# Optimization experiments

Hardware: AMD Instinct MI355X
Metric: run time of the kernel (lower is better)

Reference implementation:

```python
import jax, jax.numpy as jnp
import numpy as np

N_NODES = 50000
N_EDGES = 800000
IN_C = 32
HID = 64
N_LAYERS = 3
EDGE_HID = 128
OUT_C = 1
N_GRAPHS = 8


def setup_inputs() -> dict:
    key = jax.random.key(0)
    ks = jax.random.split(key, 32)
    x = jax.random.normal(ks[0], (N_NODES, IN_C), dtype=jnp.float32)
    # edges with src != dst so that PyG's remove_self_loops is a no-op
    src = jax.random.randint(ks[1], (N_EDGES,), 0, N_NODES)
    off = jax.random.randint(ks[2], (N_EDGES,), 1, N_NODES)
    dst = (src + off) % N_NODES
    edge_index = jnp.stack([src, dst]).astype(jnp.int32)
    batch = jnp.sort(jax.random.randint(ks[3], (N_NODES,), 0, N_GRAPHS)).astype(jnp.int32)
    inp = {"x": x, "edge_index": edge_index, "batch": batch}
    i = 4
    for l in range(N_LAYERS):
        din = IN_C if l == 0 else HID
        s = 1.0 / float(np.sqrt(din))
        inp[f"Wl{l}"] = jax.random.normal(ks[i], (din, HID), dtype=jnp.float32) * s; i += 1
        inp[f"bl{l}"] = jnp.zeros((HID,), jnp.float32)
        inp[f"Wr{l}"] = jax.random.normal(ks[i], (din, HID), dtype=jnp.float32) * s; i += 1
        inp[f"br{l}"] = jnp.zeros((HID,), jnp.float32)
        inp[f"att{l}"] = jax.random.normal(ks[i], (HID,), dtype=jnp.float32) * (1.0 / float(np.sqrt(HID))); i += 1
        inp[f"res{l}"] = jax.random.normal(ks[i], (din, HID), dtype=jnp.float32) * s; i += 1
        inp[f"bias{l}"] = jnp.zeros((HID,), jnp.float32)
        inp[f"lng{l}"] = jnp.ones((HID,), jnp.float32)
        inp[f"lnb{l}"] = jnp.zeros((HID,), jnp.float32)
    efd = 3 * HID
    inp["W1"] = jax.random.normal(ks[i], (efd, EDGE_HID), dtype=jnp.float32) * (1.0 / float(np.sqrt(efd))); i += 1
    inp["b1"] = jnp.zeros((EDGE_HID,), jnp.float32)
    inp["W2"] = jax.random.normal(ks[i], (EDGE_HID, OUT_C), dtype=jnp.float32) * (1.0 / float(np.sqrt(EDGE_HID))); i += 1
    inp["b2"] = jnp.zeros((OUT_C,), jnp.float32)
    return inp


def _gatv2_layer(x, src, dst, Wl, bl, Wr, br, att, resW, bias):
    # GATv2Conv (heads=1, share_weights=False, residual=True, add_self_loops handled by caller)
    n = x.shape[0]
    xl = x @ Wl + bl  # source transform  [N, C]
    xr = x @ Wr + br  # target transform  [N, C]
    e = jax.nn.leaky_relu(xl[src] + xr[dst], 0.2)  # [E, C]
    logits = e @ att                               # [E]
    m = jax.ops.segment_max(logits, dst, num_segments=n)
    ex = jnp.exp(logits - m[dst])
    denom = jax.ops.segment_sum(ex, dst, num_segments=n)
    alpha = ex / denom[dst]                        # edge softmax over incoming edges
    out = jax.ops.segment_sum(alpha[:, None] * xl[src], dst, num_segments=n)
    return out + x @ resW + bias


def _layernorm(h, g, b):
    mu = h.mean(-1, keepdims=True)
    var = h.var(-1, keepdims=True)
    return (h - mu) * jax.lax.rsqrt(var + 1e-5) * g + b


def reference(x, edge_index, batch,
              Wl0, bl0, Wr0, br0, att0, res0, bias0, lng0, lnb0,
              Wl1, bl1, Wr1, br1, att1, res1, bias1, lng1, lnb1,
              Wl2, bl2, Wr2, br2, att2, res2, bias2, lng2, lnb2,
              W1, b1, W2, b2):
    n = x.shape[0]
    loop = jnp.arange(n, dtype=edge_index.dtype)
    src = jnp.concatenate([edge_index[0], loop])  # add self loops
    dst = jnp.concatenate([edge_index[1], loop])
    layers = [(Wl0, bl0, Wr0, br0, att0, res0, bias0, lng0, lnb0),
              (Wl1, bl1, Wr1, br1, att1, res1, bias1, lng1, lnb1),
              (Wl2, bl2, Wr2, br2, att2, res2, bias2, lng2, lnb2)]
    h = x
    for (Wl, bl, Wr, br, att, resW, bias, g, b) in layers:
        h = _gatv2_layer(h, src, dst, Wl, bl, Wr, br, att, resW, bias)
        h = jax.nn.relu(_layernorm(h, g, b))
    node_repr = h
    gc = jax.ops.segment_sum(node_repr, batch, num_segments=N_GRAPHS)  # global_add_pool
    s, d = edge_index[0], edge_index[1]
    edge_feat = jnp.concatenate([node_repr[s], node_repr[d], gc[batch[s]]], axis=-1)  # [E, 3*HID]
    return jax.nn.relu(edge_feat @ W1 + b1) @ W2 + b2
```

## Files before the change

### kernel.cpp

```cpp
#include <hip/hip_runtime.h>
#include <math.h>

typedef float floatx2 __attribute__((ext_vector_type(2)));
typedef float floatx4 __attribute__((ext_vector_type(4)));
typedef short bf16x8 __attribute__((ext_vector_type(8)));
typedef _Float16 halfx2 __attribute__((ext_vector_type(2)));

#define NODE_MASK 0x07FFFFFF
#define LOG2E 1.4426950408889634f

__device__ __forceinline__ float wave_sum(float v){
#pragma unroll
  for (int m = 1; m < 64; m <<= 1) v += __shfl_xor(v, m, 64);
  return v;
}

__device__ __forceinline__ unsigned short bf16_of(float a){
  unsigned ua = __float_as_uint(a);
  ua = (ua + 0x7FFFu + ((ua >> 16) & 1u)) >> 16;
  return (unsigned short)ua;
}
__device__ __forceinline__ unsigned pack_bf16(float a, float b){
  unsigned ua = __float_as_uint(a), ub = __float_as_uint(b);
  ua = (ua + 0x7FFFu + ((ua >> 16) & 1u)) >> 16;
  ub = (ub + 0x7FFFu + ((ub >> 16) & 1u)) >> 16;
  return ua | (ub << 16);
}
__device__ __forceinline__ float2 unpack_bf16(unsigned p){
  float2 r;
  r.x = __uint_as_float(p << 16);
  r.y = __uint_as_float(p & 0xFFFF0000u);
  return r;
}
__device__ __forceinline__ bf16x8 to_bf16x8(float4 a, float4 b){
  bf16x8 r;
  r[0]=(short)bf16_of(a.x); r[1]=(short)bf16_of(a.y);
  r[2]=(short)bf16_of(a.z); r[3]=(short)bf16_of(a.w);
  r[4]=(short)bf16_of(b.x); r[5]=(short)bf16_of(b.y);
  r[6]=(short)bf16_of(b.z); r[7]=(short)bf16_of(b.w);
  return r;
}
__device__ __forceinline__ halfx2 f22h2(float a, float b){
  auto r = __builtin_amdgcn_cvt_pkrtz(a, b);
  return *(halfx2*)&r;
}
__device__ __forceinline__ float fdot2h(halfx2 a, halfx2 b, float c){
  return __builtin_amdgcn_fdot2(a, b, c, false);
}

__global__ __launch_bounds__(256)
void k_deg_t0(const int* __restrict__ dst, int* __restrict__ deg, int* __restrict__ rank, int e,
              const float* __restrict__ h,
              const float* __restrict__ Wl, const float* __restrict__ bl,
              const float* __restrict__ Wr, const float* __restrict__ br,
              const float* __restrict__ Wres, const float* __restrict__ bias,
              unsigned short* __restrict__ xl8, float* __restrict__ xr,
              float* __restrict__ res, int n, int nt64){
  if ((int)blockIdx.x >= nt64){
    int c = blockIdx.x - nt64;
    int i = (c*256 + (int)threadIdx.x)*4;
    if (i + 3 < e){
      int4 d4 = *(const int4*)&dst[i];
      int4 r4;
      r4.x = atomicAdd(&deg[d4.x], 1);
      r4.y = atomicAdd(&deg[d4.y], 1);
      r4.z = atomicAdd(&deg[d4.z], 1);
      r4.w = atomicAdd(&deg[d4.w], 1);
      *(int4*)&rank[i] = r4;
    } else {
      for (int j = i; j < e; ++j) rank[j] = atomicAdd(&deg[dst[j]], 1);
    }
    return;
  }
  const int K = 32, KH = 1;
  int lane = threadIdx.x & 63;
  int nt   = threadIdx.x >> 6;
  int nn = lane & 15, q = lane >> 4;
  int m0 = blockIdx.x * 64;
  if (m0 >= n) return;
  bf16x8 Af[4][KH];
#pragma unroll
  for (int t = 0; t < 4; ++t){
#pragma unroll
    for (int kh = 0; kh < KH; ++kh){
      int node = min(m0 + t*16 + nn, n - 1);
      const float* hp = h + (size_t)node*K + kh*32 + q*8;
      Af[t][kh] = to_bf16x8(*(const float4*)hp, *(const float4*)(hp + 4));
    }
  }
  int n0 = nt * 16;
  for (int sel = 0; sel < 3; ++sel){
    const float* Wp = (sel == 0) ? Wl : (sel == 1) ? Wr : Wres;
    const float* bp = (sel == 0) ? bl : (sel == 1) ? br : bias;
    bf16x8 Bf[KH];
#pragma unroll
    for (int kh = 0; kh < KH; ++kh){
#pragma unroll
      for (int j = 0; j < 8; ++j)
        Bf[kh][j] = (short)bf16_of(Wp[(kh*32 + q*8 + j)*64 + n0 + nn]);
    }
// ... 59 lines not shown
  int i = b*256 + t;
  int v = (i < n) ? (deg[i] + 1) : 0;
  sm[t] = v; __syncthreads();
#pragma unroll
  for (int off = 1; off < 256; off <<= 1){
    int x = (t >= off) ? sm[t - off] : 0;
    __syncthreads();
    sm[t] += x;
    __syncthreads();
  }
  if (i < n){
    int r = P + sm[t] - v;
    rowptr[i] = r;
    csr[r] = i | (batch[i] << 27);
  }
  if (b == nb - 1 && t == 255) rowptr[n] = P + sm[255];
  if (b == 0){
    gc[t] = 0.f;
    gc[t + 256] = 0.f;
  }
}

__global__ void k_scatter(const int* __restrict__ src, const int* __restrict__ dst,
                          const int* __restrict__ batch,
                          const int* __restrict__ rowptr, const int* __restrict__ rank,
                          int* __restrict__ csr, int* __restrict__ eidA, int e){
  int i = (blockIdx.x*blockDim.x + threadIdx.x) * 4;
  if (i + 3 < e){
    int4 s4 = *(const int4*)&src[i];
    int4 d4 = *(const int4*)&dst[i];
    int4 r4 = *(const int4*)&rank[i];
    int p0 = rowptr[d4.x] + 1 + r4.x;
    int p1 = rowptr[d4.y] + 1 + r4.y;
    int p2 = rowptr[d4.z] + 1 + r4.z;
    int p3 = rowptr[d4.w] + 1 + r4.w;
    csr[p0] = s4.x | (batch[s4.x] << 27);
    csr[p1] = s4.y | (batch[s4.y] << 27);
    csr[p2] = s4.z | (batch[s4.z] << 27);
    csr[p3] = s4.w | (batch[s4.w] << 27);
    eidA[p0] = i;
    eidA[p1] = i + 1;
    eidA[p2] = i + 2;
    eidA[p3] = i + 3;
  } else {
    for (int j = i; j < e; ++j){
      int d = dst[j], sv = src[j];
      int pos = rowptr[d] + 1 + rank[j];
      csr[pos] = sv | (batch[sv] << 27);
      eidA[pos] = j;
    }
  }
}

template<int K>
__global__ __launch_bounds__(256)
void k_node_transform(const float* __restrict__ h,
                      const float* __restrict__ Wl, const float* __restrict__ bl,
                      const float* __restrict__ Wr, const float* __restrict__ br,
                      const float* __restrict__ Wres, const float* __restrict__ bias,
                      unsigned short* __restrict__ xl8, float* __restrict__ xr,
                      float* __restrict__ res, int n){
  const int KH = K / 32;
  int lane = threadIdx.x & 63;
  int nt   = threadIdx.x >> 6;
  int nn = lane & 15, q = lane >> 4;
  int m0 = blockIdx.x * 64;
  if (m0 >= n) return;
  bf16x8 Af[4][KH];
#pragma unroll
  for (int t = 0; t < 4; ++t){
#pragma unroll
    for (int kh = 0; kh < KH; ++kh){
      int node = min(m0 + t*16 + nn, n - 1);
      const float* hp = h + (size_t)node*K + kh*32 + q*8;
      Af[t][kh] = to_bf16x8(*(const float4*)hp, *(const float4*)(hp + 4));
    }
  }
  int n0 = nt * 16;
  for (int sel = 0; sel < 3; ++sel){
    const float* Wp = (sel == 0) ? Wl : (sel == 1) ? Wr : Wres;
    const float* bp = (sel == 0) ? bl : (sel == 1) ? br : bias;
    bf16x8 Bf[KH];
#pragma unroll
    for (int kh = 0; kh < KH; ++kh){
#pragma unroll
      for (int j = 0; j < 8; ++j)
        Bf[kh][j] = (short)bf16_of(Wp[(kh*32 + q*8 + j)*64 + n0 + nn]);
    }
    float bv = bp[n0 + nn];
#pragma unroll
    for (int t = 0; t < 4; ++t){
      floatx4 acc = {bv, bv, bv, bv};
#pragma unroll
      for (int kh = 0; kh < KH; ++kh)
        acc = __builtin_amdgcn_mfma_f32_16x16x32_bf16(Af[t][kh], Bf[kh], acc, 0, 0, 0);
      int nodeb = m0 + t*16 + q*4;
      if (sel == 0){
#pragma unroll
        for (int reg = 0; reg < 4; ++reg){
          float v = acc[reg];
          float p = __shfl_xor(v, 1, 64);
          int node = nodeb + reg;
          if (!(nn & 1) && node < n)
            xl8[(size_t)node*32 + ((n0 + nn) >> 1)] =
              (unsigned short)__builtin_amdgcn_cvt_pk_fp8_f32(v, p, 0, false);
        }
      } else {
        float* op = (sel == 1) ? xr : res;
#pragma unroll
        for (int reg = 0; reg < 4; ++reg){
          int node = nodeb + reg;
          if (node < n) op[(size_t)node*64 + n0 + nn] = acc[reg];
        }
      }
    }
  }
}

__global__ void k_gat_edge(const uint2* __restrict__ xl_u2, const float* __restrict__ xr,
                           const float* __restrict__ att,
                           const float* __restrict__ lng, const float* __restrict__ lnb,
                           const int* __restrict__ rowptr, const int* __restrict__ csr,
                           float* __restrict__ hio, int n){
  int node = (blockIdx.x*blockDim.x + threadIdx.x) >> 6;
  int lane = threadIdx.x & 63;
  if (node >= n) return;
  int sub = lane >> 3;
  int l   = lane & 7;
  size_t base = (size_t)node*64 + 8*l;
  float4 xr0 = *(const float4*)&xr[base];
  float4 xr1 = *(const float4*)&xr[base + 4];
  float4 at0f = *(const float4*)&att[8*l];
  float4 at1f = *(const float4*)&att[8*l + 4];
  halfx2 xh0 = f22h2(xr0.x, xr0.y), xh1 = f22h2(xr0.z, xr0.w);
  halfx2 xh2 = f22h2(xr1.x, xr1.y), xh3 = f22h2(xr1.z, xr1.w);
  halfx2 at0 = f22h2(at0f.x*LOG2E, at0f.y*LOG2E);
  halfx2 at1 = f22h2(at0f.z*LOG2E, at0f.w*LOG2E);
  halfx2 at2 = f22h2(at1f.x*LOG2E, at1f.y*LOG2E);
  halfx2 at3 = f22h2(at1f.z*LOG2E, at1f.w*LOG2E);
  halfx2 z2  = {(_Float16)0.f, (_Float16)0.f};
  halfx2 c02 = {(_Float16)0.2f, (_Float16)0.2f};
  int p0 = rowptr[node], p1 = rowptr[node+1];
  int deg = p1 - p0;
  int sreg = csr[p0 + min(lane, deg-1)];
  int rounds = (deg + 7) >> 3;
  float dsum = 0.f;
  float a0=0.f,a1=0.f,a2=0.f,a3=0.f,a4=0.f,a5=0.f,a6=0.f,a7=0.f;
  int e0 = sub;
  bool v0 = e0 < deg;
  int s0 = __shfl(sreg, v0 ? e0 : 0, 64) & NODE_MASK;
  uint2 x0 = xl_u2[(size_t)s0*8 + l];
  int e1 = 8 + sub;
  bool v1 = e1 < deg;
  uint2 x1 = x0;
  if (rounds > 1){
    int s1 = __shfl(sreg, v1 ? e1 : 0, 64) & NODE_MASK;
    x1 = xl_u2[(size_t)s1*8 + l];
  }
  for (int r = 0; r < rounds; ++r){
    int en = 8*(r+2) + sub;
    bool vn = en < deg;
    uint2 xn = x0;
    if (r + 2 < rounds){
      int sn;
      if (en < 64) sn = __shfl(sreg, vn ? en : 0, 64);
      else         sn = csr[p0 + (vn ? en : 0)];
      sn &= NODE_MASK;
      xn = xl_u2[(size_t)sn*8 + l];
    }
    floatx2 p01 = __builtin_amdgcn_cvt_pk_f32_fp8(x0.x, false);
    floatx2 p23 = __builtin_amdgcn_cvt_pk_f32_fp8(x0.x, true);
    floatx2 p45 = __builtin_amdgcn_cvt_pk_f32_fp8(x0.y, false);
    floatx2 p67 = __builtin_amdgcn_cvt_pk_f32_fp8(x0.y, true);
    halfx2 v0h = f22h2(p01.x, p01.y) + xh0;
    halfx2 v1h = f22h2(p23.x, p23.y) + xh1;
    halfx2 v2h = f22h2(p45.x, p45.y) + xh2;
    halfx2 v3h = f22h2(p67.x, p67.y) + xh3;
    halfx2 lr0 = __builtin_elementwise_min(v0h, z2) * c02 + __builtin_elementwise_max(v0h, z2);
    halfx2 lr1 = __builtin_elementwise_min(v1h, z2) * c02 + __builtin_elementwise_max(v1h, z2);
    halfx2 lr2 = __builtin_elementwise_min(v2h, z2) * c02 + __builtin_elementwise_max(v2h, z2);
    halfx2 lr3 = __builtin_elementwise_min(v3h, z2) * c02 + __builtin_elementwise_max(v3h, z2);
    float partial = fdot2h(lr3, at3, fdot2h(lr2, at2, fdot2h(lr1, at1, fdot2h(lr0, at0, 0.f))));
#pragma unroll
    for (int mm = 1; mm < 8; mm <<= 1) partial += __shfl_xor(partial, mm, 64);
    float w = v0 ? exp2f(partial) : 0.f;
    dsum += w;
    a0 = fmaf(w, p01.x, a0);
    a1 = fmaf(w, p01.y, a1);
    a2 = fmaf(w, p23.x, a2);
    a3 = fmaf(w, p23.y, a3);
    a4 = fmaf(w, p45.x, a4);
    a5 = fmaf(w, p45.y, a5);
    a6 = fmaf(w, p67.x, a6);
    a7 = fmaf(w, p67.y, a7);
    x0 = x1; v0 = v1;
    x1 = xn; v1 = vn;
  }
#pragma unroll
  for (int off = 8; off < 64; off <<= 1){
    dsum += __shfl_xor(dsum, off, 64);
    a0 += __shfl_xor(a0, off, 64);
    a1 += __shfl_xor(a1, off, 64);
    a2 += __shfl_xor(a2, off, 64);
    a3 += __shfl_xor(a3, off, 64);
    a4 += __shfl_xor(a4, off, 64);
    a5 += __shfl_xor(a5, off, 64);
    a6 += __shfl_xor(a6, off, 64);
    a7 += __shfl_xor(a7, off, 64);
  }
  float4 r0 = *(const float4*)&hio[base];
  float4 r1 = *(const float4*)&hio[base + 4];
  float inv = __builtin_amdgcn_rcpf(dsum);
  float o0 = fmaf(a0, inv, r0.x);
  float o1 = fmaf(a1, inv, r0.y);
  float o2 = fmaf(a2, inv, r0.z);
  float o3 = fmaf(a3, inv, r0.w);
  float o4 = fmaf(a4, inv, r1.x);
  float o5 = fmaf(a5, inv, r1.y);
  float o6 = fmaf(a6, inv, r1.z);
  float o7 = fmaf(a7, inv, r1.w);
  float mean = wave_sum(o0+o1+o2+o3+o4+o5+o6+o7) * (1.f/512.f);
  float d0 = o0-mean, d1 = o1-mean, d2 = o2-mean, d3 = o3-mean;
  float d4 = o4-mean, d5 = o5-mean, d6 = o6-mean, d7 = o7-mean;
  float var = wave_sum(d0*d0+d1*d1+d2*d2+d3*d3+d4*d4+d5*d5+d6*d6+d7*d7) * (1.f/512.f);
  float rstd = rsqrtf(var + 1e-5f);
  if (sub == 0){
    float4 lg0 = *(const float4*)&lng[8*l];
    float4 lg1 = *(const float4*)&lng[8*l + 4];
    float4 lb0 = *(const float4*)&lnb[8*l];
    float4 lb1 = *(const float4*)&lnb[8*l + 4];
    float4 out0, out1;
    out0.x = fmaxf(fmaf(d0*rstd, lg0.x, lb0.x), 0.f);
    out0.y = fmaxf(fmaf(d1*rstd, lg0.y, lb0.y), 0.f);
    out0.z = fmaxf(fmaf(d2*rstd, lg0.z, lb0.z), 0.f);
    out0.w = fmaxf(fmaf(d3*rstd, lg0.w, lb0.w), 0.f);
    out1.x = fmaxf(fmaf(d4*rstd, lg1.x, lb1.x), 0.f);
    out1.y = fmaxf(fmaf(d5*rstd, lg1.y, lb1.y), 0.f);
    out1.z = fmaxf(fmaf(d6*rstd, lg1.z, lb1.z), 0.f);
    out1.w = fmaxf(fmaf(d7*rstd, lg1.w, lb1.w), 0.f);
    *(float4*)&hio[base] = out0;
    *(float4*)&hio[base + 4] = out1;
  }
}

__global__ void k_graph_proj(const float* __restrict__ gc, const float* __restrict__ W1,
                             const float* __restrict__ b1, unsigned* __restrict__ Gh){
  int g = blockIdx.x;
  int j = threadIdx.x;
  float a = b1[j];
#pragma unroll 8
  for (int k = 0; k < 64; ++k) a = fmaf(gc[g*64+k], W1[(128+k)*128 + j], a);
  float p = __shfl_xor(a, 1, 64);
  if (!(j & 1)){
    halfx2 hv = f22h2(a, p);
    Gh[g*64 + (j >> 1)] = *(unsigned*)&hv;
  }
}

__global__ __launch_bounds__(256)
void k_node_proj_pool(const float* __restrict__ nr, const float* __restrict__ W1,
                      const int* __restrict__ batch,
                      unsigned short* __restrict__ Au16, unsigned* __restrict__ Bu,
                      float* __restrict__ gc, int n, int nt64){
  int lane = threadIdx.x & 63;
  int wave = threadIdx.x >> 6;
  if ((int)blockIdx.x >= nt64){
    int wid = (blockIdx.x - nt64)*4 + wave;
    int n0 = wid*64;
    if (n0 >= n) return;
    int n1 = min(n0 + 64, n);
    int last = n1 - 1 - n0;
    int bt = batch[min(n0 + lane, n - 1)];
    int curg = __shfl(bt, 0, 64);
    float s = 0.f;
#pragma unroll
    for (int bb = 0; bb < 64; bb += 8){
      if (bb > last) break;
      float v0_ = (bb+0 <= last) ? nr[(size_t)(n0+bb+0)*64 + lane] : 0.f;
      float v1_ = (bb+1 <= last) ? nr[(size_t)(n0+bb+1)*64 + lane] : 0.f;
      float v2_ = (bb+2 <= last) ? nr[(size_t)(n0+bb+2)*64 + lane] : 0.f;
      float v3_ = (bb+3 <= last) ? nr[(size_t)(n0+bb+3)*64 + lane] : 0.f;
      float v4_ = (bb+4 <= last) ? nr[(size_t)(n0+bb+4)*64 + lane] : 0.f;
      float v5_ = (bb+5 <= last) ? nr[(size_t)(n0+bb+5)*64 + lane] : 0.f;
      float v6_ = (bb+6 <= last) ? nr[(size_t)(n0+bb+6)*64 + lane] : 0.f;
      float v7_ = (bb+7 <= last) ? nr[(size_t)(n0+bb+7)*64 + lane] : 0.f;
#pragma unroll
      for (int j = 0; j < 8; ++j){
        int g = __shfl(bt, min(bb + j, last), 64);
        if (g != curg){ atomicAdd(&gc[curg*64 + lane], s); s = 0.f; curg = g; }
        float vj = (j==0)?v0_:(j==1)?v1_:(j==2)?v2_:(j==3)?v3_:
                   (j==4)?v4_:(j==5)?v5_:(j==6)?v6_:v7_;
        s += vj;
      }
    }
    atomicAdd(&gc[curg*64 + lane], s);
    return;
  }
  int nn = lane & 15, q = lane >> 4;
  int m0 = blockIdx.x * 64;
  bf16x8 Af[4][2];
#pragma unroll
  for (int t = 0; t < 4; ++t){
#pragma unroll
    for (int kh = 0; kh < 2; ++kh){
      int node = min(m0 + t*16 + nn, n - 1);
      const float* hp = nr + (size_t)node*64 + kh*32 + q*8;
      Af[t][kh] = to_bf16x8(*(const float4*)hp, *(const float4*)(hp + 4));
    }
  }
  for (int half = 0; half < 2; ++half){
#pragma unroll
    for (int ni = 0; ni < 2; ++ni){
      int nt = wave + ni*4;
      int n0 = nt * 16;
      bf16x8 Bf[2];
#pragma unroll
      for (int kh = 0; kh < 2; ++kh){
#pragma unroll
        for (int j = 0; j < 8; ++j)
          Bf[kh][j] = (short)bf16_of(W1[(half*64 + kh*32 + q*8 + j)*128 + n0 + nn]);
      }
#pragma unroll
      for (int t = 0; t < 4; ++t){
        floatx4 acc = {0.f, 0.f, 0.f, 0.f};
#pragma unroll
        for (int kh = 0; kh < 2; ++kh)
          acc = __builtin_amdgcn_mfma_f32_16x16x32_bf16(Af[t][kh], Bf[kh], acc, 0, 0, 0);
        int nodeb = m0 + t*16 + q*4;
#pragma unroll
        for (int reg = 0; reg < 4; ++reg){
          float v = acc[reg];
          float p = __shfl_xor(v, 1, 64);
          int node = nodeb + reg;
          if (!(nn & 1) && node < n){
            int j = (n0 + nn) >> 1;
            if (half == 0)
              Au16[(size_t)node*64 + j] =
                (unsigned short)__builtin_amdgcn_cvt_pk_fp8_f32(v, p, 0, false);
            else
              Bu[(size_t)node*64 + j] = pack_bf16(v, p);
          }
        }
      }
    }
  }
}

__global__ void k_edge_out_csr(const uint4* __restrict__ Au4, const uint4* __restrict__ Bu4,
                               const unsigned* __restrict__ Gh,
                               const int* __restrict__ rowptr, const int* __restrict__ csr,
                               const int* __restrict__ eidA,
                               const float* __restrict__ W2, const float* __restrict__ b2,
                               float* __restrict__ out, int n){
  int node = (blockIdx.x*blockDim.x + threadIdx.x) >> 6;
  int lane = threadIdx.x & 63;
  if (node >= n) return;
  int sub = lane >> 3;
  int l   = lane & 7;
  int p0 = rowptr[node];
  int deg2 = rowptr[node+1] - p0 - 1;
  if (deg2 <= 0) return;
  int idx = p0 + 1 + min(lane, deg2-1);
  int sreg = csr[idx];
  int ereg = eidA[idx];
  uint4 ba = Bu4[(size_t)node*16 + 2*l];
  uint4 bb = Bu4[(size_t)node*16 + 2*l + 1];
  float2 t0 = unpack_bf16(ba.x), t1 = unpack_bf16(ba.y);
  float2 t2 = unpack_bf16(ba.z), t3 = unpack_bf16(ba.w);
  float2 t4 = unpack_bf16(bb.x), t5 = unpack_bf16(bb.y);
  float2 t6 = unpack_bf16(bb.z), t7 = unpack_bf16(bb.w);
  halfx2 bh0 = f22h2(t0.x, t0.y), bh1 = f22h2(t1.x, t1.y);
  halfx2 bh2 = f22h2(t2.x, t2.y), bh3 = f22h2(t3.x, t3.y);
  halfx2 bh4 = f22h2(t4.x, t4.y), bh5 = f22h2(t5.x, t5.y);
  halfx2 bh6 = f22h2(t6.x, t6.y), bh7 = f22h2(t7.x, t7.y);
  float4 w0 = *(const float4*)&W2[16*l];
  float4 w1 = *(const float4*)&W2[16*l + 4];
  float4 w2 = *(const float4*)&W2[16*l + 8];
  float4 w3 = *(const float4*)&W2[16*l + 12];
  halfx2 wh0 = f22h2(w0.x, w0.y), wh1 = f22h2(w0.z, w0.w);
  halfx2 wh2 = f22h2(w1.x, w1.y), wh3 = f22h2(w1.z, w1.w);
  halfx2 wh4 = f22h2(w2.x, w2.y), wh5 = f22h2(w2.z, w2.w);
  halfx2 wh6 = f22h2(w3.x, w3.y), wh7 = f22h2(w3.z, w3.w);
  halfx2 z2 = {(_Float16)0.f, (_Float16)0.f};
  float b2v = b2[0];
  int rounds = (deg2 + 7) >> 3;
  int e0 = sub;
  bool v0 = e0 < deg2;
  int q0 = v0 ? e0 : 0;
  int c0 = __shfl(sreg, q0, 64);
  int id0 = __shfl(ereg, q0, 64);
  uint4 A0 = Au4[(size_t)(c0 & NODE_MASK)*8 + l];
  int e1 = 8 + sub;
  bool v1 = e1 < deg2;
  int c1 = c0, id1 = id0; uint4 A1 = A0;
  if (rounds > 1){
    int q1 = v1 ? e1 : 0;
    c1 = __shfl(sreg, q1, 64);
// ... 8 lines not shown
      int qn = vn ? en : 0;
      if (en < 64){ cn = __shfl(sreg, qn, 64); idn = __shfl(ereg, qn, 64); }
      else        { cn = csr[p0 + 1 + qn];     idn = eidA[p0 + 1 + qn]; }
      An = Au4[(size_t)(cn & NODE_MASK)*8 + l];
    }
    int g = ((unsigned)c0) >> 27;
    const uint4* gp = (const uint4*)(Gh + g*64 + 8*l);
    uint4 g0 = gp[0], g1 = gp[1];
    halfx2 gh0 = *(halfx2*)&g0.x, gh1 = *(halfx2*)&g0.y;
    halfx2 gh2 = *(halfx2*)&g0.z, gh3 = *(halfx2*)&g0.w;
    halfx2 gh4 = *(halfx2*)&g1.x, gh5 = *(halfx2*)&g1.y;
    halfx2 gh6 = *(halfx2*)&g1.z, gh7 = *(halfx2*)&g1.w;
    floatx2 a01 = __builtin_amdgcn_cvt_pk_f32_fp8(A0.x, false);
    floatx2 a23 = __builtin_amdgcn_cvt_pk_f32_fp8(A0.x, true);
    floatx2 a45 = __builtin_amdgcn_cvt_pk_f32_fp8(A0.y, false);
    floatx2 a67 = __builtin_amdgcn_cvt_pk_f32_fp8(A0.y, true);
    floatx2 a89 = __builtin_amdgcn_cvt_pk_f32_fp8(A0.z, false);
    floatx2 aab = __builtin_amdgcn_cvt_pk_f32_fp8(A0.z, true);
    floatx2 acd = __builtin_amdgcn_cvt_pk_f32_fp8(A0.w, false);
    floatx2 aef = __builtin_amdgcn_cvt_pk_f32_fp8(A0.w, true);
    halfx2 h0 = __builtin_elementwise_max(f22h2(a01.x, a01.y) + bh0 + gh0, z2);
    halfx2 h1 = __builtin_elementwise_max(f22h2(a23.x, a23.y) + bh1 + gh1, z2);
    halfx2 h2 = __builtin_elementwise_max(f22h2(a45.x, a45.y) + bh2 + gh2, z2);
    halfx2 h3 = __builtin_elementwise_max(f22h2(a67.x, a67.y) + bh3 + gh3, z2);
    halfx2 h4 = __builtin_elementwise_max(f22h2(a89.x, a89.y) + bh4 + gh4, z2);
    halfx2 h5 = __builtin_elementwise_max(f22h2(aab.x, aab.y) + bh5 + gh5, z2);
    halfx2 h6 = __builtin_elementwise_max(f22h2(acd.x, acd.y) + bh6 + gh6, z2);
    halfx2 h7 = __builtin_elementwise_max(f22h2(aef.x, aef.y) + bh7 + gh7, z2);
    float part = fdot2h(h7, wh7, fdot2h(h6, wh6, fdot2h(h5, wh5, fdot2h(h4, wh4,
                 fdot2h(h3, wh3, fdot2h(h2, wh2, fdot2h(h1, wh1, fdot2h(h0, wh0, 0.f))))))));
#pragma unroll
    for (int mm = 1; mm < 8; mm <<= 1) part += __shfl_xor(part, mm, 64);
    if (l == 0 && v0) out[id0] = part + b2v;
    c0 = c1; id0 = id1; A0 = A1; v0 = v1;
    c1 = cn; id1 = idn; A1 = An; v1 = vn;
  }
}

extern "C" void kernel_launch(void* const* d_in, const int* in_sizes, int n_in,
                              void* d_out, int out_size, void* d_ws, size_t ws_size,
                              hipStream_t stream){
  const float* x     = (const float*)d_in[0];
  const int*   ei    = (const int*)d_in[1];
  const int*   batch = (const int*)d_in[2];
  const int N = in_sizes[2];
  const int E = in_sizes[1] / 2;
  const int* src = ei;
  const int* dst = ei + E;

  unsigned* W = (unsigned*)d_ws;
  const size_t N16 = (size_t)N * 16;
  const size_t N32 = (size_t)N * 32;
  const size_t N64 = (size_t)N * 64;
  unsigned short* xl8 = (unsigned short*)W;
  float* xr = (float*)(W + N16);
  float* hE = (float*)(W + N16 + N64);
  float* hD = (float*)(W + N16 + 2*N64);
  unsigned short* Au16 = (unsigned short*)W;
  unsigned* Bu = W + N32;
  int* rowptr = (int*)(W + N16 + 3*N64);
  int* deg    = rowptr + (N + 16);
  int* csr    = deg + N;
  int* rank   = csr + (N + E);
  int* eidA   = rank + E;
  float* gc   = (float*)(eidA + (N + E));
  unsigned* Gh = (unsigned*)(gc + 512);
  int* bsum   = (int*)(Gh + 512);

  const int NB = (N + 255) / 256;
  const int NT64 = (N + 63) / 64;
  const int ECH = (E/4 + 255) / 256;

  (void)hipMemsetAsync(deg, 0, (size_t)N*4, stream);
  const float* Wl0   = (const float*)d_in[3];
  const float* bl0   = (const float*)d_in[4];
  const float* Wr0   = (const float*)d_in[5];
  const float* br0   = (const float*)d_in[6];
  const float* Wres0 = (const float*)d_in[8];
  const float* bias0 = (const float*)d_in[9];
  k_deg_t0 <<<NT64 + ECH, 256, 0, stream>>>(dst, deg, rank, E,
                                            x, Wl0, bl0, Wr0, br0, Wres0, bias0,
                                            xl8, xr, hD, N, NT64);
  k_scan_reduce<<<NB, 256, 0, stream>>>(deg, bsum, N);
  k_scan_apply <<<NB, 256, 0, stream>>>(deg, bsum, rowptr, csr, batch, gc, N, NB);
  k_scatter    <<<ECH, 256, 0, stream>>>(src, dst, batch, rowptr, rank, csr, eidA, E);

  const float* h = hD;
  float* hn = hD;
  for (int l = 0; l < 3; ++l){
    const float* Wl   = (const float*)d_in[3 + 9*l + 0];
    const float* bl   = (const float*)d_in[3 + 9*l + 1];
    const float* Wr   = (const float*)d_in[3 + 9*l + 2];
    const float* br   = (const float*)d_in[3 + 9*l + 3];
    const float* att  = (const float*)d_in[3 + 9*l + 4];
    const float* Wres = (const float*)d_in[3 + 9*l + 5];
    const float* bias = (const float*)d_in[3 + 9*l + 6];
    const float* lng  = (const float*)d_in[3 + 9*l + 7];
    const float* lnb  = (const float*)d_in[3 + 9*l + 8];
    if (l > 0)
      k_node_transform<64><<<NT64, 256, 0, stream>>>(h, Wl, bl, Wr, br, Wres, bias, xl8, xr, hn, N);
    k_gat_edge<<<(N+3)/4, 256, 0, stream>>>((const uint2*)xl8, xr, att, lng, lnb, rowptr, csr, hn, N);
    h = hn;
    hn = (l == 0) ? hE : hD;
  }

  const float* W1 = (const float*)d_in[30];
  const float* b1 = (const float*)d_in[31];
  const float* W2 = (const float*)d_in[32];
  const float* b2 = (const float*)d_in[33];

  int pool_waves = (N + 63) / 64;
  int poolB = (pool_waves + 3) / 4;
  k_node_proj_pool<<<NT64 + poolB, 256, 0, stream>>>(hD, W1, batch, Au16, Bu, gc, N, NT64);
  k_graph_proj<<<8, 128, 0, stream>>>(gc, W1, b1, Gh);
  k_edge_out_csr<<<(N+3)/4, 256, 0, stream>>>((const uint4*)Au16, (const uint4*)Bu, Gh,
                                              rowptr, csr, eidA, W2, b2, (float*)d_out, N);
}
```

Measured before the change: 392.6 us.

## Fuse GAT edge aggregation with next-layer node transform per 64-node block

Merges each layer's edge attention/aggregation kernel with the following node transform (and the final layer with the W1 projection and pooling) into one kernel per block of 64 nodes. Each wave processes 16 nodes serially, then after a block barrier the block runs the MFMA transform on the freshly normalized rows, which should still be in cache. Double-buffered xl/xr buffers avoid read/write races across blocks. This cuts kernel launches and a global round-trip of h. In exchange there are far fewer waves per node (one wave loops over 16 nodes, versus one node per wave before), which reduces parallelism and latency hiding for the gather-heavy edge phase.

Result: slower. 452.3 us (+15.2%).

```diff
diff --git a/kernel.cpp b/kernel.cpp
--- a/kernel.cpp
+++ b/kernel.cpp
@@ -46,6 +46,118 @@
 }
 __device__ __forceinline__ float fdot2h(halfx2 a, halfx2 b, float c){
   return __builtin_amdgcn_fdot2(a, b, c, false);
+}
+
+__device__ __forceinline__ void gat_node(int node, int lane, int sub, int l,
+    const uint2* __restrict__ xl_u2, const float* __restrict__ xr,
+    const int* __restrict__ rowptr, const int* __restrict__ csr,
+    float* __restrict__ hio,
+    halfx2 at0, halfx2 at1, halfx2 at2, halfx2 at3,
+    float4 lg0, float4 lg1, float4 lb0, float4 lb1){
+  halfx2 z2  = {(_Float16)0.f, (_Float16)0.f};
+  halfx2 c02 = {(_Float16)0.2f, (_Float16)0.2f};
+  size_t base = (size_t)node*64 + 8*l;
+  float4 xr0 = *(const float4*)&xr[base];
+  float4 xr1 = *(const float4*)&xr[base + 4];
+  halfx2 xh0 = f22h2(xr0.x, xr0.y), xh1 = f22h2(xr0.z, xr0.w);
+  halfx2 xh2 = f22h2(xr1.x, xr1.y), xh3 = f22h2(xr1.z, xr1.w);
+  int p0 = rowptr[node], p1 = rowptr[node+1];
+  int deg = p1 - p0;
+  int sreg = csr[p0 + min(lane, deg-1)];
+  int rounds = (deg + 7) >> 3;
+  float dsum = 0.f;
+  float a0=0.f,a1=0.f,a2=0.f,a3=0.f,a4=0.f,a5=0.f,a6=0.f,a7=0.f;
+  int e0 = sub;
+  bool v0 = e0 < deg;
+  int s0 = __shfl(sreg, v0 ? e0 : 0, 64) & NODE_MASK;
+  uint2 x0 = xl_u2[(size_t)s0*8 + l];
+  int e1 = 8 + sub;
+  bool v1 = e1 < deg;
+  uint2 x1 = x0;
+  if (rounds > 1){
+    int s1 = __shfl(sreg, v1 ? e1 : 0, 64) & NODE_MASK;
+    x1 = xl_u2[(size_t)s1*8 + l];
+  }
+  for (int r = 0; r < rounds; ++r){
+    int en = 8*(r+2) + sub;
+    bool vn = en < deg;
+    uint2 xn = x0;
+    if (r + 2 < rounds){
+      int sn;
+      if (en < 64) sn = __shfl(sreg, vn ? en : 0, 64);
+      else         sn = csr[p0 + (vn ? en : 0)];
+      sn &= NODE_MASK;
+      xn = xl_u2[(size_t)sn*8 + l];
+    }
+    floatx2 p01 = __builtin_amdgcn_cvt_pk_f32_fp8(x0.x, false);
+    floatx2 p23 = __builtin_amdgcn_cvt_pk_f32_fp8(x0.x, true);
+    floatx2 p45 = __builtin_amdgcn_cvt_pk_f32_fp8(x0.y, false);
+    floatx2 p67 = __builtin_amdgcn_cvt_pk_f32_fp8(x0.y, true);
+    halfx2 v0h = f22h2(p01.x, p01.y) + xh0;
+    halfx2 v1h = f22h2(p23.x, p23.y) + xh1;
+    halfx2 v2h = f22h2(p45.x, p45.y) + xh2;
+    halfx2 v3h = f22h2(p67.x, p67.y) + xh3;
+    halfx2 lr0 = __builtin_elementwise_min(v0h, z2) * c02 + __builtin_elementwise_max(v0h, z2);
+    halfx2 lr1 = __builtin_elementwise_min(v1h, z2) * c02 + __builtin_elementwise_max(v1h, z2);
+    halfx2 lr2 = __builtin_elementwise_min(v2h, z2) * c02 + __builtin_elementwise_max(v2h, z2);
+    halfx2 lr3 = __builtin_elementwise_min(v3h, z2) * c02 + __builtin_elementwise_max(v3h, z2);
+    float partial = fdot2h(lr3, at3, fdot2h(lr2, at2, fdot2h(lr1, at1, fdot2h(lr0, at0, 0.f))));
+#pragma unroll
+    for (int mm = 1; mm < 8; mm <<= 1) partial += __shfl_xor(partial, mm, 64);
+    float w = v0 ? exp2f(partial) : 0.f;
+    dsum += w;
+    a0 = fmaf(w, p01.x, a0);
+    a1 = fmaf(w, p01.y, a1);
+    a2 = fmaf(w, p23.x, a2);
+    a3 = fmaf(w, p23.y, a3);
+    a4 = fmaf(w, p45.x, a4);
+    a5 = fmaf(w, p45.y, a5);
+    a6 = fmaf(w, p67.x, a6);
+    a7 = fmaf(w, p67.y, a7);
+    x0 = x1; v0 = v1;
+    x1 = xn; v1 = vn;
+  }
+#pragma unroll
+  for (int off = 8; off < 64; off <<= 1){
+    dsum += __shfl_xor(dsum, off, 64);
+    a0 += __shfl_xor(a0, off, 64);
+    a1 += __shfl_xor(a1, off, 64);
+    a2 += __shfl_xor(a2, off, 64);
+    a3 += __shfl_xor(a3, off, 64);
+    a4 += __shfl_xor(a4, off, 64);
+    a5 += __shfl_xor(a5, off, 64);
+    a6 += __shfl_xor(a6, off, 64);
+    a7 += __shfl_xor(a7, off, 64);
+  }
+  float4 r0 = *(const float4*)&hio[base];
+  float4 r1 = *(const float4*)&hio[base + 4];
+  float inv = __builtin_amdgcn_rcpf(dsum);
+  float o0 = fmaf(a0, inv, r0.x);
+  float o1 = fmaf(a1, inv, r0.y);
+  float o2 = fmaf(a2, inv, r0.z);
+  float o3 = fmaf(a3, inv, r0.w);
+  float o4 = fmaf(a4, inv, r1.x);
+  float o5 = fmaf(a5, inv, r1.y);
+  float o6 = fmaf(a6, inv, r1.z);
+  float o7 = fmaf(a7, inv, r1.w);
+  float mean = wave_sum(o0+o1+o2+o3+o4+o5+o6+o7) * (1.f/512.f);
+  float d0 = o0-mean, d1 = o1-mean, d2 = o2-mean, d3 = o3-mean;
+  float d4 = o4-mean, d5 = o5-mean, d6 = o6-mean, d7 = o7-mean;
+  float var = wave_sum(d0*d0+d1*d1+d2*d2+d3*d3+d4*d4+d5*d5+d6*d6+d7*d7) * (1.f/512.f);
+  float rstd = rsqrtf(var + 1e-5f);
+  if (sub == 0){
+    float4 out0, out1;
+    out0.x = fmaxf(fmaf(d0*rstd, lg0.x, lb0.x), 0.f);
+    out0.y = fmaxf(fmaf(d1*rstd, lg0.y, lb0.y), 0.f);
+    out0.z = fmaxf(fmaf(d2*rstd, lg0.z, lb0.z), 0.f);
+    out0.w = fmaxf(fmaf(d3*rstd, lg0.w, lb0.w), 0.f);
+    out1.x = fmaxf(fmaf(d4*rstd, lg1.x, lb1.x), 0.f);
+    out1.y = fmaxf(fmaf(d5*rstd, lg1.y, lb1.y), 0.f);
+    out1.z = fmaxf(fmaf(d6*rstd, lg1.z, lb1.z), 0.f);
+    out1.w = fmaxf(fmaf(d7*rstd, lg1.w, lb1.w), 0.f);
+    *(float4*)&hio[base] = out0;
+    *(float4*)&hio[base + 4] = out1;
+  }
 }
 
 __global__ __launch_bounds__(256)
@@ -211,194 +323,197 @@
   }
 }
 
-template<int K>
 __global__ __launch_bounds__(256)
-void k_node_transform(const float* __restrict__ h,
-                      const float* __restrict__ Wl, const float* __restrict__ bl,
-                      const float* __restrict__ Wr, const float* __restrict__ br,
-                      const float* __restrict__ Wres, const float* __restrict__ bias,
-                      unsigned short* __restrict__ xl8, float* __restrict__ xr,
-                      float* __restrict__ res, int n){
-  const int KH = K / 32;
+void k_gat_tr(const uint2* __restrict__ xl_in, const float* __restrict__ xr_in,
+              const float* __restrict__ att, const float* __restrict__ lng,
+              const float* __restrict__ lnb,
+              const int* __restrict__ rowptr, const int* __restrict__ csr,
+              float* __restrict__ hio,
+              const float* __restrict__ Wl, const float* __restrict__ bl,
+              const float* __restrict__ Wr, const float* __restrict__ br,
+              const float* __restrict__ Wres, const float* __restrict__ bias,
+              unsigned short* __restrict__ xl_out, float* __restrict__ xr_out,
+              float* __restrict__ res_out,
+              int n){
   int lane = threadIdx.x & 63;
-  int nt   = threadIdx.x >> 6;
-  int nn = lane & 15, q = lane >> 4;
+  int wave = threadIdx.x >> 6;
+  int sub = lane >> 3;
+  int l   = lane & 7;
+  int l8  = l * 8;
   int m0 = blockIdx.x * 64;
   if (m0 >= n) return;
-  bf16x8 Af[4][KH];
-#pragma unroll
-  for (int t = 0; t < 4; ++t){
-#pragma unroll
-    for (int kh = 0; kh < KH; ++kh){
-      int node = min(m0 + t*16 + nn, n - 1);
-      const float* hp = h + (size_t)node*K + kh*32 + q*8;
-      Af[t][kh] = to_bf16x8(*(const float4*)hp, *(const float4*)(hp + 4));
-    }
-  }
-  int n0 = nt * 16;
-  for (int sel = 0; sel < 3; ++sel){
-    const float* Wp = (sel == 0) ? Wl : (sel == 1) ? Wr : Wres;
-    const float* bp = (sel == 0) ? bl : (sel == 1) ? br : bias;
-    bf16x8 Bf[KH];
-#pragma unroll
-    for (int kh = 0; kh < KH; ++kh){
-#pragma unroll
-      for (int j = 0; j < 8; ++j)
-        Bf[kh][j] = (short)bf16_of(Wp[(kh*32 + q*8 + j)*64 + n0 + nn]);
-    }
-    float bv = bp[n0 + nn];
+  {
+    float4 at0f = *(const float4*)&att[l8];
+    float4 at1f = *(const float4*)&att[l8 + 4];
+    halfx2 at0 = f22h2(at0f.x*LOG2E, at0f.y*LOG2E);
+    halfx2 at1 = f22h2(at0f.z*LOG2E, at0f.w*LOG2E);
+    halfx2 at2 = f22h2(at1f.x*LOG2E, at1f.y*LOG2E);
+    halfx2 at3 = f22h2(at1f.z*LOG2E, at1f.w*LOG2E);
+    float4 lg0 = *(const float4*)&lng[l8];
+    float4 lg1 = *(const float4*)&lng[l8 + 4];
+    float4 lb0 = *(const float4*)&lnb[l8];
+    float4 lb1 = *(const float4*)&lnb[l8 + 4];
+    int nb0 = m0 + wave*16;
+    for (int i = 0; i < 16; ++i){
+      int node = nb0 + i;
+      if (node < n)
+        gat_node(node, lane, sub, l, xl_in, xr_in, rowptr, csr, hio,
+                 at0, at1, at2, at3, lg0, lg1, lb0, lb1);
+    }
+  }
+  __syncthreads();
+  {
+    int nn = lane & 15, q = lane >> 4;
+    bf16x8 Af[4][2];
 #pragma unroll
     for (int t = 0; t < 4; ++t){
-      floatx4 acc = {bv, bv, bv, bv};
-#pragma unroll
-      for (int kh = 0; kh < KH; ++kh)
-        acc = __builtin_amdgcn_mfma_f32_16x16x32_bf16(Af[t][kh], Bf[kh], acc, 0, 0, 0);
-      int nodeb = m0 + t*16 + q*4;
-      if (sel == 0){
-#pragma unroll
-        for (int reg = 0; reg < 4; ++reg){
-          float v = acc[reg];
-          float p = __shfl_xor(v, 1, 64);
-          int node = nodeb + reg;
-          if (!(nn & 1) && node < n)
-            xl8[(size_t)node*32 + ((n0 + nn) >> 1)] =
-              (unsigned short)__builtin_amdgcn_cvt_pk_fp8_f32(v, p, 0, false);
-        }
-      } else {
-        float* op = (sel == 1) ? xr : res;
-#pragma unroll
-        for (int reg = 0; reg < 4; ++reg){
-          int node = nodeb + reg;
-          if (node < n) op[(size_t)node*64 + n0 + nn] = acc[reg];
+#pragma unroll
+      for (int kh = 0; kh < 2; ++kh){
+        int node = min(m0 + t*16 + nn, n - 1);
+        const float* hp = hio + (size_t)node*64 + kh*32 + q*8;
+        Af[t][kh] = to_bf16x8(*(const float4*)hp, *(const float4*)(hp + 4));
+      }
+    }
+    int n0 = wave * 16;
+    for (int sel = 0; sel < 3; ++sel){
+      const float* Wp = (sel == 0) ? Wl : (sel == 1) ? Wr : Wres;
+      const float* bp = (sel == 0) ? bl : (sel == 1) ? br : bias;
+      bf16x8 Bf[2];
+#pragma unroll
+      for (int kh = 0; kh < 2; ++kh){
+#pragma unroll
+        for (int j = 0; j < 8; ++j)
+          Bf[kh][j] = (short)bf16_of(Wp[(kh*32 + q*8 + j)*64 + n0 + nn]);
+      }
+      float bv = bp[n0 + nn];
+#pragma unroll
+      for (int t = 0; t < 4; ++t){
+        floatx4 acc = {bv, bv, bv, bv};
+#pragma unroll
+        for (int kh = 0; kh < 2; ++kh)
+          acc = __builtin_amdgcn_mfma_f32_16x16x32_bf16(Af[t][kh], Bf[kh], acc, 0, 0, 0);
+        int nodeb = m0 + t*16 + q*4;
+        if (sel == 0){
+#pragma unroll
+          for (int reg = 0; reg < 4; ++reg){
+            float v = acc[reg];
+            float p = __shfl_xor(v, 1, 64);
+            int node = nodeb + reg;
+            if (!(nn & 1) && node < n)
+              xl_out[(size_t)node*32 + ((n0 + nn) >> 1)] =
+                (unsigned short)__builtin_amdgcn_cvt_pk_fp8_f32(v, p, 0, false);
+          }
+        } else {
+          float* op = (sel == 1) ? xr_out : res_out;
+#pragma unroll
+          for (int reg = 0; reg < 4; ++reg){
+            int node = nodeb + reg;
+            if (node < n) op[(size_t)node*64 + n0 + nn] = acc[reg];
+          }
         }
       }
     }
   }
 }
 
-__global__ void k_gat_edge(const uint2* __restrict__ xl_u2, const float* __restrict__ xr,
-                           const float* __restrict__ att,
-                           const float* __restrict__ lng, const float* __restrict__ lnb,
-                           const int* __restrict__ rowptr, const int* __restrict__ csr,
-                           float* __restrict__ hio, int n){
-  int node = (blockIdx.x*blockDim.x + threadIdx.x) >> 6;
+__global__ __launch_bounds__(256)
+void k_gat_pp(const uint2* __restrict__ xl_in, const float* __restrict__ xr_in,
+              const float* __restrict__ att, const float* __restrict__ lng,
+              const float* __restrict__ lnb,
+              const int* __restrict__ rowptr, const int* __restrict__ csr,
+              float* __restrict__ hio,
+              const float* __restrict__ W1, const int* __restrict__ batch,
+              unsigned short* __restrict__ Au16, unsigned* __restrict__ Bu,
+              float* __restrict__ gc, int n){
   int lane = threadIdx.x & 63;
-  if (node >= n) return;
+  int wave = threadIdx.x >> 6;
   int sub = lane >> 3;
   int l   = lane & 7;
-  size_t base = (size_t)node*64 + 8*l;
-  float4 xr0 = *(const float4*)&xr[base];
-  float4 xr1 = *(const float4*)&xr[base + 4];
-  float4 at0f = *(const float4*)&att[8*l];
-  float4 at1f = *(const float4*)&att[8*l + 4];
-  halfx2 xh0 = f22h2(xr0.x, xr0.y), xh1 = f22h2(xr0.z, xr0.w);
-  halfx2 xh2 = f22h2(xr1.x, xr1.y), xh3 = f22h2(xr1.z, xr1.w);
-  halfx2 at0 = f22h2(at0f.x*LOG2E, at0f.y*LOG2E);
-  halfx2 at1 = f22h2(at0f.z*LOG2E, at0f.w*LOG2E);
-  halfx2 at2 = f22h2(at1f.x*LOG2E, at1f.y*LOG2E);
-  halfx2 at3 = f22h2(at1f.z*LOG2E, at1f.w*LOG2E);
-  halfx2 z2  = {(_Float16)0.f, (_Float16)0.f};
-  halfx2 c02 = {(_Float16)0.2f, (_Float16)0.2f};
-  int p0 = rowptr[node], p1 = rowptr[node+1];
-  int deg = p1 - p0;
-  int sreg = csr[p0 + min(lane, deg-1)];
-  int rounds = (deg + 7) >> 3;
-  float dsum = 0.f;
-  float a0=0.f,a1=0.f,a2=0.f,a3=0.f,a4=0.f,a5=0.f,a6=0.f,a7=0.f;
-  int e0 = sub;
-  bool v0 = e0 < deg;
-  int s0 = __shfl(sreg, v0 ? e0 : 0, 64) & NODE_MASK;
-  uint2 x0 = xl_u2[(size_t)s0*8 + l];
-  int e1 = 8 + sub;
-  bool v1 = e1 < deg;
-  uint2 x1 = x0;
-  if (rounds > 1){
-    int s1 = __shfl(sreg, v1 ? e1 : 0, 64) & NODE_MASK;
-    x1 = xl_u2[(size_t)s1*8 + l];
-  }
-  for (int r = 0; r < rounds; ++r){
-    int en = 8*(r+2) + sub;
-    bool vn = en < deg;
-    uint2 xn = x0;
-    if (r + 2 < rounds){
-      int sn;
-      if (en < 64) sn = __shfl(sreg, vn ? en : 0, 64);
-      else         sn = csr[p0 + (vn ? en : 0)];
-      sn &= NODE_MASK;
-      xn = xl_u2[(size_t)sn*8 + l];
-    }
-    floatx2 p01 = __builtin_amdgcn_cvt_pk_f32_fp8(x0.x, false);
-    floatx2 p23 = __builtin_amdgcn_cvt_pk_f32_fp8(x0.x, true);
-    floatx2 p45 = __builtin_amdgcn_cvt_pk_f32_fp8(x0.y, false);
-    floatx2 p67 = __builtin_amdgcn_cvt_pk_f32_fp8(x0.y, true);
-    halfx2 v0h = f22h2(p01.x, p01.y) + xh0;
-    halfx2 v1h = f22h2(p23.x, p23.y) + xh1;
-    halfx2 v2h = f22h2(p45.x, p45.y) + xh2;
-    halfx2 v3h = f22h2(p67.x, p67.y) + xh3;
-    halfx2 lr0 = __builtin_elementwise_min(v0h, z2) * c02 + __builtin_elementwise_max(v0h, z2);
-    halfx2 lr1 = __builtin_elementwise_min(v1h, z2) * c02 + __builtin_elementwise_max(v1h, z2);
-    halfx2 lr2 = __builtin_elementwise_min(v2h, z2) * c02 + __builtin_elementwise_max(v2h, z2);
-    halfx2 lr3 = __builtin_elementwise_min(v3h, z2) * c02 + __builtin_elementwise_max(v3h, z2);
-    float partial = fdot2h(lr3, at3, fdot2h(lr2, at2, fdot2h(lr1, at1, fdot2h(lr0, at0, 0.f))));
-#pragma unroll
-    for (int mm = 1; mm < 8; mm <<= 1) partial += __shfl_xor(partial, mm, 64);
-    float w = v0 ? exp2f(partial) : 0.f;
-    dsum += w;
-    a0 = fmaf(w, p01.x, a0);
-    a1 = fmaf(w, p01.y, a1);
-    a2 = fmaf(w, p23.x, a2);
-    a3 = fmaf(w, p23.y, a3);
-    a4 = fmaf(w, p45.x, a4);
-    a5 = fmaf(w, p45.y, a5);
-    a6 = fmaf(w, p67.x, a6);
-    a7 = fmaf(w, p67.y, a7);
-    x0 = x1; v0 = v1;
-    x1 = xn; v1 = vn;
-  }
-#pragma unroll
-  for (int off = 8; off < 64; off <<= 1){
-    dsum += __shfl_xor(dsum, off, 64);
-    a0 += __shfl_xor(a0, off, 64);
-    a1 += __shfl_xor(a1, off, 64);
-    a2 += __shfl_xor(a2, off, 64);
-    a3 += __shfl_xor(a3, off, 64);
-    a4 += __shfl_xor(a4, off, 64);
-    a5 += __shfl_xor(a5, off, 64);
-    a6 += __shfl_xor(a6, off, 64);
-    a7 += __shfl_xor(a7, off, 64);
-  }
-  float4 r0 = *(const float4*)&hio[base];
-  float4 r1 = *(const float4*)&hio[base + 4];
-  float inv = __builtin_amdgcn_rcpf(dsum);
-  float o0 = fmaf(a0, inv, r0.x);
-  float o1 = fmaf(a1, inv, r0.y);
-  float o2 = fmaf(a2, inv, r0.z);
-  float o3 = fmaf(a3, inv, r0.w);
-  float o4 = fmaf(a4, inv, r1.x);
-  float o5 = fmaf(a5, inv, r1.y);
-  float o6 = fmaf(a6, inv, r1.z);
-  float o7 = fmaf(a7, inv, r1.w);
-  float mean = wave_sum(o0+o1+o2+o3+o4+o5+o6+o7) * (1.f/512.f);
-  float d0 = o0-mean, d1 = o1-mean, d2 = o2-mean, d3 = o3-mean;
-  float d4 = o4-mean, d5 = o5-mean, d6 = o6-mean, d7 = o7-mean;
-  float var = wave_sum(d0*d0+d1*d1+d2*d2+d3*d3+d4*d4+d5*d5+d6*d6+d7*d7) * (1.f/512.f);
-  float rstd = rsqrtf(var + 1e-5f);
-  if (sub == 0){
-    float4 lg0 = *(const float4*)&lng[8*l];
-    float4 lg1 = *(const float4*)&lng[8*l + 4];
-    float4 lb0 = *(const float4*)&lnb[8*l];
-    float4 lb1 = *(const float4*)&lnb[8*l + 4];
-    float4 out0, out1;
-    out0.x = fmaxf(fmaf(d0*rstd, lg0.x, lb0.x), 0.f);
-    out0.y = fmaxf(fmaf(d1*rstd, lg0.y, lb0.y), 0.f);
-    out0.z = fmaxf(fmaf(d2*rstd, lg0.z, lb0.z), 0.f);
-    out0.w = fmaxf(fmaf(d3*rstd, lg0.w, lb0.w), 0.f);
-    out1.x = fmaxf(fmaf(d4*rstd, lg1.x, lb1.x), 0.f);
-    out1.y = fmaxf(fmaf(d5*rstd, lg1.y, lb1.y), 0.f);
-    out1.z = fmaxf(fmaf(d6*rstd, lg1.z, lb1.z), 0.f);
-    out1.w = fmaxf(fmaf(d7*rstd, lg1.w, lb1.w), 0.f);
-    *(float4*)&hio[base] = out0;
-    *(float4*)&hio[base + 4] = out1;
+  int l8  = l * 8;
+  int m0 = blockIdx.x * 64;
+  if (m0 >= n) return;
+  {
+    float4 at0f = *(const float4*)&att[l8];
+    float4 at1f = *(const float4*)&att[l8 + 4];
+    halfx2 at0 = f22h2(at0f.x*LOG2E, at0f.y*LOG2E);
+    halfx2 at1 = f22h2(at0f.z*LOG2E, at0f.w*LOG2E);
+    halfx2 at2 = f22h2(at1f.x*LOG2E, at1f.y*LOG2E);
+    halfx2 at3 = f22h2(at1f.z*LOG2E, at1f.w*LOG2E);
+    float4 lg0 = *(const float4*)&lng[l8];
+    float4 lg1 = *(const float4*)&lng[l8 + 4];
+    float4 lb0 = *(const float4*)&lnb[l8];
+    float4 lb1 = *(const float4*)&lnb[l8 + 4];
+    int nb0 = m0 + wave*16;
+    for (int i = 0; i < 16; ++i){
+      int node = nb0 + i;
+      if (node < n)
+        gat_node(node, lane, sub, l, xl_in, xr_in, rowptr, csr, hio,
+                 at0, at1, at2, at3, lg0, lg1, lb0, lb1);
+    }
+  }
+  __syncthreads();
+  {
+    int base = m0 + wave*16;
+    int lim = min(base + 16, n) - base;
+    if (lim > 0){
+      int curg = batch[base];
+      float s = 0.f;
+      for (int i = 0; i < lim; ++i){
+        int g = batch[base + i];
+        if (g != curg){ atomicAdd(&gc[curg*64 + lane], s); s = 0.f; curg = g; }
+        s += hio[(size_t)(base + i)*64 + lane];
+      }
+      atomicAdd(&gc[curg*64 + lane], s);
+    }
+  }
+  {
+    int nn = lane & 15, q = lane >> 4;
+    bf16x8 Af[4][2];
+#pragma unroll
+    for (int t = 0; t < 4; ++t){
+#pragma unroll
+      for (int kh = 0; kh < 2; ++kh){
+        int node = min(m0 + t*16 + nn, n - 1);
+        const float* hp = hio + (size_t)node*64 + kh*32 + q*8;
+        Af[t][kh] = to_bf16x8(*(const float4*)hp, *(const float4*)(hp + 4));
+      }
+    }
+    for (int half = 0; half < 2; ++half){
+#pragma unroll
+      for (int ni = 0; ni < 2; ++ni){
+        int nt = wave + ni*4;
+        int n0 = nt * 16;
+        bf16x8 Bf[2];
+#pragma unroll
+        for (int kh = 0; kh < 2; ++kh){
+#pragma unroll
+          for (int j = 0; j < 8; ++j)
+            Bf[kh][j] = (short)bf16_of(W1[(half*64 + kh*32 + q*8 + j)*128 + n0 + nn]);
+        }
+#pragma unroll
+        for (int t = 0; t < 4; ++t){
+          floatx4 acc = {0.f, 0.f, 0.f, 0.f};
+#pragma unroll
+          for (int kh = 0; kh < 2; ++kh)
+            acc = __builtin_amdgcn_mfma_f32_16x16x32_bf16(Af[t][kh], Bf[kh], acc, 0, 0, 0);
+          int nodeb = m0 + t*16 + q*4;
+#pragma unroll
+          for (int reg = 0; reg < 4; ++reg){
+            float v = acc[reg];
+            float p = __shfl_xor(v, 1, 64);
+            int node = nodeb + reg;
+            if (!(nn & 1) && node < n){
+              int j = (n0 + nn) >> 1;
+              if (half == 0)
+                Au16[(size_t)node*64 + j] =
+                  (unsigned short)__builtin_amdgcn_cvt_pk_fp8_f32(v, p, 0, false);
+              else
+                Bu[(size_t)node*64 + j] = pack_bf16(v, p);
+            }
+          }
+        }
+      }
+    }
   }
 }
 
@@ -413,95 +528,6 @@
   if (!(j & 1)){
     halfx2 hv = f22h2(a, p);
     Gh[g*64 + (j >> 1)] = *(unsigned*)&hv;
-  }
-}
-
-__global__ __launch_bounds__(256)
-void k_node_proj_pool(const float* __restrict__ nr, const float* __restrict__ W1,
-                      const int* __restrict__ batch,
-                      unsigned short* __restrict__ Au16, unsigned* __restrict__ Bu,
-                      float* __restrict__ gc, int n, int nt64){
-  int lane = threadIdx.x & 63;
-  int wave = threadIdx.x >> 6;
-  if ((int)blockIdx.x >= nt64){
-    int wid = (blockIdx.x - nt64)*4 + wave;
-    int n0 = wid*64;
-    if (n0 >= n) return;
-    int n1 = min(n0 + 64, n);
-    int last = n1 - 1 - n0;
-    int bt = batch[min(n0 + lane, n - 1)];
-    int curg = __shfl(bt, 0, 64);
-    float s = 0.f;
-#pragma unroll
-    for (int bb = 0; bb < 64; bb += 8){
-      if (bb > last) break;
-      float v0_ = (bb+0 <= last) ? nr[(size_t)(n0+bb+0)*64 + lane] : 0.f;
-      float v1_ = (bb+1 <= last) ? nr[(size_t)(n0+bb+1)*64 + lane] : 0.f;
-      float v2_ = (bb+2 <= last) ? nr[(size_t)(n0+bb+2)*64 + lane] : 0.f;
-      float v3_ = (bb+3 <= last) ? nr[(size_t)(n0+bb+3)*64 + lane] : 0.f;
-      float v4_ = (bb+4 <= last) ? nr[(size_t)(n0+bb+4)*64 + lane] : 0.f;
-      float v5_ = (bb+5 <= last) ? nr[(size_t)(n0+bb+5)*64 + lane] : 0.f;
-      float v6_ = (bb+6 <= last) ? nr[(size_t)(n0+bb+6)*64 + lane] : 0.f;
-      float v7_ = (bb+7 <= last) ? nr[(size_t)(n0+bb+7)*64 + lane] : 0.f;
-#pragma unroll
-      for (int j = 0; j < 8; ++j){
-        int g = __shfl(bt, min(bb + j, last), 64);
-        if (g != curg){ atomicAdd(&gc[curg*64 + lane], s); s = 0.f; curg = g; }
-        float vj = (j==0)?v0_:(j==1)?v1_:(j==2)?v2_:(j==3)?v3_:
-                   (j==4)?v4_:(j==5)?v5_:(j==6)?v6_:v7_;
-        s += vj;
-      }
-    }
-    atomicAdd(&gc[curg*64 + lane], s);
-    return;
-  }
-  int nn = lane & 15, q = lane >> 4;
-  int m0 = blockIdx.x * 64;
-  bf16x8 Af[4][2];
-#pragma unroll
-  for (int t = 0; t < 4; ++t){
-#pragma unroll
-    for (int kh = 0; kh < 2; ++kh){
-      int node = min(m0 + t*16 + nn, n - 1);
-      const float* hp = nr + (size_t)node*64 + kh*32 + q*8;
-      Af[t][kh] = to_bf16x8(*(const float4*)hp, *(const float4*)(hp + 4));
-    }
-  }
-  for (int half = 0; half < 2; ++half){
-#pragma unroll
-    for (int ni = 0; ni < 2; ++ni){
-      int nt = wave + ni*4;
-      int n0 = nt * 16;
-      bf16x8 Bf[2];
-#pragma unroll
-      for (int kh = 0; kh < 2; ++kh){
-#pragma unroll
-        for (int j = 0; j < 8; ++j)
-          Bf[kh][j] = (short)bf16_of(W1[(half*64 + kh*32 + q*8 + j)*128 + n0 + nn]);
-      }
-#pragma unroll
-      for (int t = 0; t < 4; ++t){
-        floatx4 acc = {0.f, 0.f, 0.f, 0.f};
-#pragma unroll
-        for (int kh = 0; kh < 2; ++kh)
-          acc = __builtin_amdgcn_mfma_f32_16x16x32_bf16(Af[t][kh], Bf[kh], acc, 0, 0, 0);
-        int nodeb = m0 + t*16 + q*4;
-#pragma unroll
-        for (int reg = 0; reg < 4; ++reg){
-          float v = acc[reg];
-          float p = __shfl_xor(v, 1, 64);
-          int node = nodeb + reg;
-          if (!(nn & 1) && node < n){
-            int j = (n0 + nn) >> 1;
-            if (half == 0)
-              Au16[(size_t)node*64 + j] =
-                (unsigned short)__builtin_amdgcn_cvt_pk_fp8_f32(v, p, 0, false);
-            else
-              Bu[(size_t)node*64 + j] = pack_bf16(v, p);
-          }
-        }
-      }
-    }
   }
 }
 
@@ -616,13 +642,15 @@
   const size_t N16 = (size_t)N * 16;
   const size_t N32 = (size_t)N * 32;
   const size_t N64 = (size_t)N * 64;
-  unsigned short* xl8 = (unsigned short*)W;
-  float* xr = (float*)(W + N16);
-  float* hE = (float*)(W + N16 + N64);
-  float* hD = (float*)(W + N16 + 2*N64);
-  unsigned short* Au16 = (unsigned short*)W;
-  unsigned* Bu = W + N32;
-  int* rowptr = (int*)(W + N16 + 3*N64);
+  unsigned short* xl8_a = (unsigned short*)W;
+  unsigned short* xl8_b = (unsigned short*)(W + N16);
+  float* xr_a = (float*)(W + 2*N16);
+  float* xr_b = (float*)(W + 2*N16 + N64);
+  float* hD   = (float*)(W + 2*N16 + 2*N64);
+  float* hE   = (float*)(W + 2*N16 + 3*N64);
+  unsigned short* Au16 = (unsigned short*)(W + 2*N16 + 4*N64);
+  unsigned* Bu = W + 2*N16 + 4*N64 + N32;
+  int* rowptr = (int*)(W + 2*N16 + 5*N64 + N32);
   int* deg    = rowptr + (N + 16);
   int* csr    = deg + N;
   int* rank   = csr + (N + E);
@@ -644,38 +672,32 @@
   const float* bias0 = (const float*)d_in[9];
   k_deg_t0 <<<NT64 + ECH, 256, 0, stream>>>(dst, deg, rank, E,
                                             x, Wl0, bl0, Wr0, br0, Wres0, bias0,
-                                            xl8, xr, hD, N, NT64);
+                                            xl8_a, xr_a, hD, N, NT64);
   k_scan_reduce<<<NB, 256, 0, stream>>>(deg, bsum, N);
   k_scan_apply <<<NB, 256, 0, stream>>>(deg, bsum, rowptr, csr, batch, gc, N, NB);
   k_scatter    <<<ECH, 256, 0, stream>>>(src, dst, batch, rowptr, rank, csr, eidA, E);
 
-  const float* h = hD;
-  float* hn = hD;
-  for (int l = 0; l < 3; ++l){
-    const float* Wl   = (const float*)d_in[3 + 9*l + 0];
-    const float* bl   = (const float*)d_in[3 + 9*l + 1];
-    const float* Wr   = (const float*)d_in[3 + 9*l + 2];
-    const float* br   = (const float*)d_in[3 + 9*l + 3];
-    const float* att  = (const float*)d_in[3 + 9*l + 4];
-    const float* Wres = (const float*)d_in[3 + 9*l + 5];
-    const float* bias = (const float*)d_in[3 + 9*l + 6];
-    const float* lng  = (const float*)d_in[3 + 9*l + 7];
-    const float* lnb  = (const float*)d_in[3 + 9*l + 8];
-    if (l > 0)
-      k_node_transform<64><<<NT64, 256, 0, stream>>>(h, Wl, bl, Wr, br, Wres, bias, xl8, xr, hn, N);
-    k_gat_edge<<<(N+3)/4, 256, 0, stream>>>((const uint2*)xl8, xr, att, lng, lnb, rowptr, csr, hn, N);
-    h = hn;
-    hn = (l == 0) ? hE : hD;
-  }
-
+  k_gat_tr<<<NT64, 256, 0, stream>>>((const uint2*)xl8_a, xr_a,
+      (const float*)d_in[7], (const float*)d_in[10], (const float*)d_in[11],
+      rowptr, csr, hD,
+      (const float*)d_in[12], (const float*)d_in[13], (const float*)d_in[14],
+      (const float*)d_in[15], (const float*)d_in[17], (const float*)d_in[18],
+      xl8_b, xr_b, hE, N);
+  k_gat_tr<<<NT64, 256, 0, stream>>>((const uint2*)xl8_b, xr_b,
+      (const float*)d_in[16], (const float*)d_in[19], (const float*)d_in[20],
+      rowptr, csr, hE,
+      (const float*)d_in[21], (const float*)d_in[22], (const float*)d_in[23],
+      (const float*)d_in[24], (const float*)d_in[26], (const float*)d_in[27],
+      xl8_a, xr_a, hD, N);
   const float* W1 = (const float*)d_in[30];
   const float* b1 = (const float*)d_in[31];
   const float* W2 = (const float*)d_in[32];
   const float* b2 = (const float*)d_in[33];
-
-  int pool_waves = (N + 63) / 64;
-  int poolB = (pool_waves + 3) / 4;
-  k_node_proj_pool<<<NT64 + poolB, 256, 0, stream>>>(hD, W1, batch, Au16, Bu, gc, N, NT64);
+  k_gat_pp<<<NT64, 256, 0, stream>>>((const uint2*)xl8_a, xr_a,
+      (const float*)d_in[25], (const float*)d_in[28], (const float*)d_in[29],
+      rowptr, csr, hD,
+      W1, batch, Au16, Bu, gc, N);
+
   k_graph_proj<<<8, 128, 0, stream>>>(gc, W1, b1, Gh);
   k_edge_out_csr<<<(N+3)/4, 256, 0, stream>>>((const uint4*)Au16, (const uint4*)Bu, Gh,
                                               rowptr, csr, eidA, W2, b2, (float*)d_out, N);
```
